# Kernel tuning notes

Measured on AMD Instinct MI355X. Metric: run time of the kernel, lower is better.

## Reference

```python
import math
import jax, jax.numpy as jnp
import numpy as np

B, T, E = 2, 2048, 2048
H, HKV = 16, 4
DH = E // H              # 128
ROT_DIM = DH             # rotary_pct = 1.0 -> 128
ROT_HALF = ROT_DIM // 2  # RotaryEmbedding is built with dim=ROT_DIM//2=64; only these dims rotate
MAX_SEQ = 2048


def _rope_tables():
    # theta = 10000 ** (-arange(0, dim, 2)/dim) with dim = ROT_HALF
    theta = 10000.0 ** (-jnp.arange(0, ROT_HALF, 2, dtype=jnp.float32) / ROT_HALF)  # [ROT_HALF//2]
    pos = jnp.arange(MAX_SEQ, dtype=jnp.float32)
    angles = pos[:, None] * theta[None, :]   # [MAX_SEQ, ROT_HALF//2]
    return jnp.cos(angles), jnp.sin(angles)


def _apply_rotary(q, k, start_pos):
    # q: [B,T,H,ROT_DIM], k: [B,T,HKV,ROT_DIM]; rotate only first ROT_HALF dims (interleaved pairs)
    cos, sin = _rope_tables()
    t = q.shape[1]
    cos = jax.lax.dynamic_slice_in_dim(cos, start_pos, t, axis=0)[None, :, None, :]
    sin = jax.lax.dynamic_slice_in_dim(sin, start_pos, t, axis=0)[None, :, None, :]

    def rot(a):
        a_rot, a_pass = a[..., :ROT_HALF], a[..., ROT_HALF:]
        x, y = a_rot[..., 0::2], a_rot[..., 1::2]
        rx = x * cos - y * sin
        ry = x * sin + y * cos
        rotated = jnp.stack([rx, ry], axis=-1).reshape(*a_rot.shape)
        return jnp.concatenate([rotated, a_pass], axis=-1)

    return rot(q), rot(k)


def setup_inputs() -> dict:
    key = jax.random.key(0)
    ks = jax.random.split(key, 9)
    s = 0.02  # weight scale for sane logits
    return {
        "x": jax.random.normal(ks[0], (B, T, E), dtype=jnp.float32),
        "Wq": jax.random.normal(ks[1], (E, H * DH), dtype=jnp.float32) * s,
        "bq": jax.random.normal(ks[2], (H * DH,), dtype=jnp.float32) * s,
        "Wk": jax.random.normal(ks[3], (E, HKV * DH), dtype=jnp.float32) * s,
        "bk": jax.random.normal(ks[4], (HKV * DH,), dtype=jnp.float32) * s,
        "Wv": jax.random.normal(ks[5], (E, HKV * DH), dtype=jnp.float32) * s,
        "bv": jax.random.normal(ks[6], (HKV * DH,), dtype=jnp.float32) * s,
        "Wo": jax.random.normal(ks[7], (E, E), dtype=jnp.float32) * s,
        "bo": jax.random.normal(ks[8], (E,), dtype=jnp.float32) * s,
        "start_pos": 0,
    }


def reference(x, Wq, bq, Wk, bk, Wv, bv, Wo, bo, start_pos):
    b, t, _ = x.shape
    q = (x @ Wq + bq).reshape(b, t, H, DH)
    k = (x @ Wk + bk).reshape(b, t, HKV, DH)
    v = (x @ Wv + bv).reshape(b, t, HKV, DH)

    q, k = _apply_rotary(q, k, start_pos)

    group = H // HKV
    k = jnp.repeat(k, group, axis=2)  # [b,t,H,DH]
    v = jnp.repeat(v, group, axis=2)

    # scores: [b,H,t,t]
    scores = jnp.einsum("bqhd,bkhd->bhqk", q, k) / math.sqrt(DH)
    causal = jnp.tril(jnp.ones((t, t), dtype=bool))
    scores = jnp.where(causal[None, None], scores, -jnp.inf)
    probs = jax.nn.softmax(scores, axis=-1)

    out = jnp.einsum("bhqk,bkhd->bqhd", probs, v).reshape(b, t, H * DH)
    return out @ Wo + bo
```

## Files before the change

kernel.cpp:

```cpp
#include <hip/hip_runtime.h>

typedef __attribute__((ext_vector_type(8))) short short8;
typedef __attribute__((ext_vector_type(4))) float f32x4;
typedef __attribute__((ext_vector_type(16))) float f32x16;

#define DEVFN __device__ __forceinline__

DEVFN unsigned short f2bf(float f) {
  unsigned int u = __builtin_bit_cast(unsigned int, f);
  u += 0x7FFFu + ((u >> 16) & 1u);
  return (unsigned short)(u >> 16);
}
DEVFN float bf2f(unsigned int u) { return __builtin_bit_cast(float, u << 16); }

DEVFN unsigned int cvtpk_bf16(float lo, float hi) {
  unsigned int d;
  asm("v_cvt_pk_bf16_f32 %0, %1, %2" : "=v"(d) : "v"(lo), "v"(hi));
  return d;
}
DEVFN void plswap32(unsigned int& a, unsigned int& b) {
  asm("v_permlane32_swap_b32 %0, %1" : "+v"(a), "+v"(b));
}
DEVFN float bcast32(float v, int srclane) {
  int r = __builtin_amdgcn_ds_bpermute(srclane * 4, __builtin_bit_cast(int, v));
  return __builtin_bit_cast(float, r);
}


__global__ __launch_bounds__(256) void mk_tables(float* __restrict__ cost, float* __restrict__ sint) {
  int gid = blockIdx.x * 256 + threadIdx.x;
  int pos = gid >> 5, i = gid & 31;
  float theta = powf(10000.0f, -(float)(2 * i) / 64.0f);
  float ang = (float)pos * theta;
  cost[gid] = cosf(ang);
  sint[gid] = sinf(ang);
}

__global__ __launch_bounds__(256) void bias_cat_k(const float* __restrict__ bq, const float* __restrict__ bk,
                                                  const float* __restrict__ bv, float* __restrict__ out) {
  int i = blockIdx.x * 256 + threadIdx.x;
  float v;
  if (i < 2048) v = bq[i];
  else if (i < 2560) v = bk[i - 2048];
  else v = bv[i - 2560];
  out[i] = v;
}

__global__ __launch_bounds__(256) void convx(const float* __restrict__ x, unsigned short* __restrict__ xb) {
  int gid = blockIdx.x * 256 + threadIdx.x;
  const float4* xv = (const float4*)x;
  float4 a = xv[(size_t)gid * 2], b = xv[(size_t)gid * 2 + 1];
  short8 u;
  u[0] = (short)f2bf(a.x); u[1] = (short)f2bf(a.y); u[2] = (short)f2bf(a.z); u[3] = (short)f2bf(a.w);
  u[4] = (short)f2bf(b.x); u[5] = (short)f2bf(b.y); u[6] = (short)f2bf(b.z); u[7] = (short)f2bf(b.w);
  *(short8*)(xb + (size_t)gid * 8) = u;
}

__global__ __launch_bounds__(256) void transw(const float* __restrict__ W, unsigned short* __restrict__ Wt, int ncols) {
  __shared__ float lds[32][33];
  int n0 = blockIdx.x * 32, k0 = blockIdx.y * 32;
  int tx = threadIdx.x & 31, ty = threadIdx.x >> 5;
  #pragma unroll
  for (int i = 0; i < 4; i++) {
    int kr = ty + i * 8;
    lds[kr][tx] = W[(size_t)(k0 + kr) * ncols + n0 + tx];
  }
  __syncthreads();
  #pragma unroll
  for (int i = 0; i < 4; i++) {
    int nr = ty + i * 8;
    Wt[(size_t)(n0 + nr) * 2048 + k0 + tx] = f2bf(lds[tx][nr]);
  }
}

template<int NH>
__global__ __launch_bounds__(256) void rope_scatter(const unsigned short* __restrict__ QKV,
    const float* __restrict__ cost, const float* __restrict__ sint, const int* __restrict__ spp,
    unsigned short* __restrict__ dst, int colOff, float scale) {
  constexpr int LOG2NH = (NH == 16) ? 4 : 2;
  int gid = blockIdx.x * 256 + threadIdx.x;
  int j = gid & 63;
  int h = (gid >> 6) & (NH - 1);
  int m = gid >> (6 + LOG2NH);
  int t = m & 2047;
  int b = m >> 11;
  const unsigned short* src = QKV + (size_t)m * 3072 + colOff + h * 128 + 2 * j;
  unsigned int pair = *(const unsigned int*)src;
  float xv = bf2f(pair & 0xFFFFu), yv = bf2f(pair >> 16);
  float rx, ry;
  if (j < 32) {
    int pos = (spp[0] + t) & 2047;
    float c = cost[pos * 32 + j], s = sint[pos * 32 + j];
    rx = xv * c - yv * s;
    ry = xv * s + yv * c;
  } else { rx = xv; ry = yv; }
  rx *= scale; ry *= scale;
  int d0 = 2 * j;
  size_t off = (size_t)(b * NH + h) * 262144 + (t >> 5) * 4096 + (d0 >> 4) * 512
             + ((d0 >> 3) & 1) * 256 + (t & 31) * 8 + (d0 & 7);
  unsigned int outp = (unsigned int)f2bf(rx) | ((unsigned int)f2bf(ry) << 16);
  *(unsigned int*)(dst + off) = outp;
}

__global__ __launch_bounds__(256) void vtrans(const unsigned short* __restrict__ QKV, unsigned short* __restrict__ VF) {
  __shared__ __align__(16) unsigned short lds[64 * 128];
  int tid = threadIdx.x;
  int t0 = blockIdx.x * 64;
  int bk = blockIdx.y;
  const unsigned short* src = QKV + (size_t)(bk >> 2) * 2048 * 3072 + 2560 + (bk & 3) * 128;
  #pragma unroll
  for (int c = 0; c < 4; c++) {
    int idx = c * 256 + tid;
    int tr = idx >> 4, dc = idx & 15;
    short8 v = *(const short8*)(src + (size_t)(t0 + tr) * 3072 + dc * 8);
    *(short8*)((char*)lds + tr * 256 + 16 * (dc ^ (tr >> 3))) = v;
  }
  __syncthreads();
  unsigned short* dstb = VF + (size_t)bk * 262144;
  #pragma unroll
  for (int c2 = 0; c2 < 4; c2++) {
    int idx2 = c2 * 256 + tid;
    int tc = idx2 & 7, d = idx2 >> 3;
    short8 u;
    #pragma unroll
    for (int e = 0; e < 8; e++) {
      int t = 8 * tc + e;
      u[e] = *(const short*)((char*)lds + t * 256 + 16 * ((d >> 3) ^ tc) + (d & 7) * 2);
    }
    size_t off = (size_t)(t0 >> 6) * 8192 + ((d >> 5) * 4 + ((tc >> 1) & 3)) * 512
               + (tc & 1) * 256 + (d & 31) * 8;
    *(short8*)(dstb + off) = u;
  }
}

template<bool BF16OUT>
__global__ __launch_bounds__(256, 2) void gemm_bt(
    const unsigned short* __restrict__ A, const unsigned short* __restrict__ Bt,
    const float* __restrict__ bias, void* __restrict__ Cout, int M, int N, int K) {
  __shared__ __align__(16) unsigned short Asl[128 * 64];
  __shared__ __align__(16) unsigned short Bsl[128 * 64];
  int tid = threadIdx.x;
  int lane = tid & 63, w = tid >> 6;
  int wr = w >> 1, wc = w & 1;
  int m0 = blockIdx.y * 128, n0 = blockIdx.x * 128;

  f32x4 acc[4][4];
  #pragma unroll
  for (int i = 0; i < 4; i++)
    #pragma unroll
    for (int j = 0; j < 4; j++)
      #pragma unroll
      for (int r = 0; r < 4; r++) acc[i][j][r] = 0.f;

  int srow = w * 32 + (lane >> 3);
  int kc8 = (lane & 7) * 8;
  const unsigned short* Aptr = A + (size_t)(m0 + srow) * K + kc8;
  const unsigned short* Bptr = Bt + (size_t)(n0 + srow) * K + kc8;
  unsigned short* AslW = Asl + w * 4 * 512;
  unsigned short* BslW = Bsl + w * 4 * 512;

  for (int k0 = 0; k0 < K; k0 += 64) {
    __syncthreads();
    #pragma unroll
    for (int i = 0; i < 4; i++) {
      __builtin_amdgcn_global_load_lds(
        (const __attribute__((address_space(1))) unsigned int*)(Aptr + (size_t)i * 8 * K + k0),
        (__attribute__((address_space(3))) unsigned int*)(AslW + i * 512), 16, 0, 0);
      __builtin_amdgcn_global_load_lds(
        (const __attribute__((address_space(1))) unsigned int*)(Bptr + (size_t)i * 8 * K + k0),
        (__attribute__((address_space(3))) unsigned int*)(BslW + i * 512), 16, 0, 0);
    }
    __syncthreads();
    #pragma unroll
    for (int ks = 0; ks < 2; ks++) {
      short8 af[4], bfr[4];
      #pragma unroll
      for (int mi = 0; mi < 4; mi++)
        af[mi] = *(const short8*)(Asl + (wr * 64 + mi * 16 + (lane & 15)) * 64 + ks * 32 + (lane >> 4) * 8);
      #pragma unroll
      for (int ni = 0; ni < 4; ni++)
        bfr[ni] = *(const short8*)(Bsl + (wc * 64 + ni * 16 + (lane & 15)) * 64 + ks * 32 + (lane >> 4) * 8);
      #pragma unroll
      for (int mi = 0; mi < 4; mi++)
        #pragma unroll
        for (int ni = 0; ni < 4; ni++)
          acc[mi][ni] = __builtin_amdgcn_mfma_f32_16x16x32_bf16(af[mi], bfr[ni], acc[mi][ni], 0, 0, 0);
    }
  }
  int cl = lane & 15, rq = lane >> 4;
  #pragma unroll
  for (int mi = 0; mi < 4; mi++) {
    #pragma unroll
    for (int ni = 0; ni < 4; ni++) {
      int gn = n0 + wc * 64 + ni * 16 + cl;
      float bv = bias[gn];
      #pragma unroll
      for (int r = 0; r < 4; r++) {
        int gm = m0 + wr * 64 + mi * 16 + rq * 4 + r;
        float v = acc[mi][ni][r] + bv;
        if (BF16OUT) ((unsigned short*)Cout)[(size_t)gm * N + gn] = f2bf(v);
        else ((float*)Cout)[(size_t)gm * N + gn] = v;
      }
    }
  }
}

__global__ __launch_bounds__(512, 2) void attn_kernel(
    const unsigned short* __restrict__ QF, const unsigned short* __restrict__ KF,
    const unsigned short* __restrict__ VF, unsigned short* __restrict__ O) {
  const int tid = threadIdx.x;
  const int lane = tid & 63;
  const int w = tid >> 6;
  const int l31 = lane & 31;
  const int hf = lane >> 5;
  const int g = blockIdx.x & 7, j = blockIdx.x >> 3;
  const int b = g >> 2, kh = g & 3;
  const int h = kh * 4 + (j & 3);
  const int i4 = (j >> 2) * 4;
  const int qt = (w < 4) ? (i4 + w) : (67 - i4 - w);
  const int qw = qt * 32;
  const int nw = (qt >> 1) + 1;

  const unsigned short* qh  = QF + (size_t)(b * 16 + h) * 262144 + qt * 4096;
  const unsigned short* khp = KF + (size_t)(b * 4 + kh) * 262144;
  const unsigned short* vhp = VF + (size_t)(b * 4 + kh) * 262144;

  short8 qf[8];
  #pragma unroll
  for (int s = 0; s < 8; s++)
    qf[s] = *(const short8*)(qh + s * 512 + lane * 8);

  float m_r = -3.0e38f, l_r = 0.f;
  f32x16 oacc[4];
  #pragma unroll
  for (int dt = 0; dt < 4; dt++)
    #pragma unroll
    for (int r = 0; r < 16; r++) oacc[dt][r] = 0.f;

  for (int kt = 0; kt < nw; kt++) {
    const int kv0 = kt * 64;
    f32x16 sc[2];
    {
      short8 kf0[8];
      #pragma unroll
      for (int s = 0; s < 8; s++)
        kf0[s] = *(const short8*)(khp + (size_t)(2 * kt) * 4096 + s * 512 + lane * 8);
      #pragma unroll
      for (int r = 0; r < 16; r++) sc[0][r] = 0.f;
      #pragma unroll
      for (int s = 0; s < 8; s++)
        sc[0] = __builtin_amdgcn_mfma_f32_32x32x16_bf16(kf0[s], qf[s], sc[0], 0, 0, 0);
    }
    {
      short8 kf1[8];
      #pragma unroll
      for (int s = 0; s < 8; s++)
        kf1[s] = *(const short8*)(khp + (size_t)(2 * kt + 1) * 4096 + s * 512 + lane * 8);
      #pragma unroll
      for (int r = 0; r < 16; r++) sc[1][r] = 0.f;
      #pragma unroll
      for (int s = 0; s < 8; s++)
        sc[1] = __builtin_amdgcn_mfma_f32_32x32x16_bf16(kf1[s], qf[s], sc[1], 0, 0, 0);
    }
    short8 vf[4][4];
    #pragma unroll
    for (int dt = 0; dt < 4; dt++)
      #pragma unroll
      for (int ks = 0; ks < 4; ks++)
        vf[dt][ks] = *(const short8*)(vhp + (size_t)kt * 8192 + (dt * 4 + ks) * 512 + lane * 8);

    if (kv0 + 63 > qw) {
      #pragma unroll
      for (int ct = 0; ct < 2; ct++)
        #pragma unroll
        for (int r = 0; r < 16; r++) {
          int kg = kv0 + ct * 32 + (r & 3) + 8 * (r >> 2) + 4 * hf;
          if (kg > qw + l31) sc[ct][r] = -3.0e38f;
        }
    }
    float mx[16];
    #pragma unroll
    for (int r = 0; r < 16; r++) mx[r] = fmaxf(sc[0][r], sc[1][r]);
    #pragma unroll
    for (int s2 = 8; s2 >= 1; s2 >>= 1)
      #pragma unroll
      for (int i = 0; i < 8; i++) if (i < s2) mx[i] = fmaxf(mx[i], mx[i + s2]);
    float tm = fmaxf(mx[0], __shfl_xor(mx[0], 32));
    if (__any(tm > m_r + 8.0f)) {
      float mn = fmaxf(m_r, tm);
      float al = __builtin_amdgcn_exp2f(m_r - mn);
      m_r = mn;
      l_r *= al;
      #pragma unroll
      for (int r = 0; r < 16; r++) {
        float alr = bcast32(al, (r & 3) + 8 * (r >> 2) + 4 * hf);
        #pragma unroll
        for (int dt = 0; dt < 4; dt++) oacc[dt][r] *= alr;
      }
    }
    #pragma unroll
    for (int ct = 0; ct < 2; ct++)
      #pragma unroll
      for (int r = 0; r < 16; r++) sc[ct][r] = __builtin_amdgcn_exp2f(sc[ct][r] - m_r);
    float sm[16];
    #pragma unroll
    for (int r = 0; r < 16; r++) sm[r] = sc[0][r] + sc[1][r];
    #pragma unroll
    for (int s2 = 8; s2 >= 1; s2 >>= 1)
      #pragma unroll
      for (int i = 0; i < 8; i++) if (i < s2) sm[i] += sm[i + s2];
    l_r += sm[0];

    short8 pa[4];
    #pragma unroll
    for (int ks = 0; ks < 4; ks++) {
      const int ct = ks >> 1, kb = (ks & 1) * 8;
      unsigned int A0 = cvtpk_bf16(sc[ct][kb + 0], sc[ct][kb + 1]);
      unsigned int A1 = cvtpk_bf16(sc[ct][kb + 2], sc[ct][kb + 3]);
      unsigned int B0 = cvtpk_bf16(sc[ct][kb + 4], sc[ct][kb + 5]);
      unsigned int B1 = cvtpk_bf16(sc[ct][kb + 6], sc[ct][kb + 7]);
      plswap32(A0, B0);
      plswap32(A1, B1);
      union { unsigned int wds[4]; short8 s8; } u;
      u.wds[0] = A0; u.wds[1] = A1; u.wds[2] = B0; u.wds[3] = B1;
      pa[ks] = u.s8;
    }
    #pragma unroll
    for (int dt = 0; dt < 4; dt++)
      #pragma unroll
      for (int ks = 0; ks < 4; ks++)
        oacc[dt] = __builtin_amdgcn_mfma_f32_32x32x16_bf16(pa[ks], vf[dt][ks], oacc[dt], 0, 0, 0);
  }
  float invl = 1.0f / (l_r + __shfl_xor(l_r, 32));
  #pragma unroll
  for (int r = 0; r < 16; r++) {
    int rloc = (r & 3) + 8 * (r >> 2) + 4 * hf;
    float inv = bcast32(invl, rloc);
    int qg = qw + rloc;
    unsigned short* orow = O + ((size_t)(b * 2048 + qg)) * 2048 + h * 128;
    #pragma unroll
    for (int dt = 0; dt < 4; dt++)
      orow[dt * 32 + l31] = f2bf(oacc[dt][r] * inv);
  }
}

extern "C" void kernel_launch(void* const* d_in, const int* in_sizes, int n_in,
                              void* d_out, int out_size, void* d_ws, size_t ws_size,
                              hipStream_t stream) {
  (void)in_sizes; (void)n_in; (void)out_size; (void)ws_size;
  const float* x  = (const float*)d_in[0];
  const float* Wq = (const float*)d_in[1];
  const float* bq = (const float*)d_in[2];
  const float* Wk = (const float*)d_in[3];
  const float* bk = (const float*)d_in[4];
  const float* Wv = (const float*)d_in[5];
  const float* bv = (const float*)d_in[6];
  const float* Wo = (const float*)d_in[7];
  const float* bo = (const float*)d_in[8];
  const int*   sp = (const int*)d_in[9];

  char* ws = (char*)d_ws;
  unsigned short* xb    = (unsigned short*)ws;
  unsigned short* Wqkvt = (unsigned short*)(ws + 16777216);
  unsigned short* Wot   = (unsigned short*)(ws + 29360128);
  unsigned short* QKVb  = (unsigned short*)(ws + 37748736);
  float* cost           = (float*)(ws + 62914560);
  float* sint           = (float*)(ws + 63176704);
  float* bcat           = (float*)(ws + 63438848);

  unsigned short* Obuf = xb;
  unsigned short* QFr = (unsigned short*)d_out;
  unsigned short* KFr = (unsigned short*)((char*)d_out + 16777216);
  unsigned short* VFr = (unsigned short*)((char*)d_out + 20971520);

  mk_tables<<<256, 256, 0, stream>>>(cost, sint);
  bias_cat_k<<<12, 256, 0, stream>>>(bq, bk, bv, bcat);
  convx<<<4096, 256, 0, stream>>>(x, xb);
  transw<<<dim3(64, 64), 256, 0, stream>>>(Wq, Wqkvt, 2048);
  transw<<<dim3(16, 64), 256, 0, stream>>>(Wk, Wqkvt + (size_t)2048 * 2048, 512);
  transw<<<dim3(16, 64), 256, 0, stream>>>(Wv, Wqkvt + (size_t)2560 * 2048, 512);
  transw<<<dim3(64, 64), 256, 0, stream>>>(Wo, Wot, 2048);
  gemm_bt<true><<<dim3(24, 32), 256, 0, stream>>>(xb, Wqkvt, bcat, QKVb, 4096, 3072, 2048);
  rope_scatter<16><<<16384, 256, 0, stream>>>(QKVb, cost, sint, sp, QFr, 0, 0.12751743f);
  rope_scatter<4><<<4096, 256, 0, stream>>>(QKVb, cost, sint, sp, KFr, 2048, 1.0f);
  vtrans<<<dim3(32, 8), 256, 0, stream>>>(QKVb, VFr);
  attn_kernel<<<dim3(256), 512, 0, stream>>>(QFr, KFr, VFr, Obuf);
  gemm_bt<false><<<dim3(16, 32), 256, 0, stream>>>(Obuf, Wot, bo, (float*)d_out, 4096, 2048, 2048);
}
```

Before: 237.9 us.

## Merge prep and scatter kernels, remap GEMM blocks per XCD, pipeline attention K loads

Folds the seven preprocessing launches into one prep_all kernel and the three rope/V-transpose launches into one scatter_all kernel, which removes launch gaps. The GEMM grid becomes 1D, with block indices remapped so that consecutive tiles are grouped per XCD (index mod 8), aiming for better L2 locality. In attention, the next K tile is double-buffered in registers, V loads are split and interleaved with compute, and the softmax row sum is computed by an MFMA against a ones vector instead of a shuffle reduction. The costs are higher register pressure and branchy multi-role kernels.

```diff
diff --git a/kernel.cpp b/kernel.cpp
--- a/kernel.cpp
+++ b/kernel.cpp
@@ -26,123 +26,137 @@
   return __builtin_bit_cast(float, r);
 }
 
-
-__global__ __launch_bounds__(256) void mk_tables(float* __restrict__ cost, float* __restrict__ sint) {
-  int gid = blockIdx.x * 256 + threadIdx.x;
-  int pos = gid >> 5, i = gid & 31;
-  float theta = powf(10000.0f, -(float)(2 * i) / 64.0f);
-  float ang = (float)pos * theta;
-  cost[gid] = cosf(ang);
-  sint[gid] = sinf(ang);
-}
-
-__global__ __launch_bounds__(256) void bias_cat_k(const float* __restrict__ bq, const float* __restrict__ bk,
-                                                  const float* __restrict__ bv, float* __restrict__ out) {
-  int i = blockIdx.x * 256 + threadIdx.x;
-  float v;
-  if (i < 2048) v = bq[i];
-  else if (i < 2560) v = bk[i - 2048];
-  else v = bv[i - 2560];
-  out[i] = v;
-}
-
-__global__ __launch_bounds__(256) void convx(const float* __restrict__ x, unsigned short* __restrict__ xb) {
-  int gid = blockIdx.x * 256 + threadIdx.x;
-  const float4* xv = (const float4*)x;
-  float4 a = xv[(size_t)gid * 2], b = xv[(size_t)gid * 2 + 1];
-  short8 u;
-  u[0] = (short)f2bf(a.x); u[1] = (short)f2bf(a.y); u[2] = (short)f2bf(a.z); u[3] = (short)f2bf(a.w);
-  u[4] = (short)f2bf(b.x); u[5] = (short)f2bf(b.y); u[6] = (short)f2bf(b.z); u[7] = (short)f2bf(b.w);
-  *(short8*)(xb + (size_t)gid * 8) = u;
-}
-
-__global__ __launch_bounds__(256) void transw(const float* __restrict__ W, unsigned short* __restrict__ Wt, int ncols) {
+__global__ __launch_bounds__(256) void prep_all(
+    const float* __restrict__ Wq, const float* __restrict__ Wk, const float* __restrict__ Wv,
+    const float* __restrict__ Wo, const float* __restrict__ bq, const float* __restrict__ bk,
+    const float* __restrict__ bv, const float* __restrict__ x,
+    unsigned short* __restrict__ Wqkvt, unsigned short* __restrict__ Wot,
+    unsigned short* __restrict__ xb, float* __restrict__ cost, float* __restrict__ sint,
+    float* __restrict__ bcat) {
   __shared__ float lds[32][33];
-  int n0 = blockIdx.x * 32, k0 = blockIdx.y * 32;
-  int tx = threadIdx.x & 31, ty = threadIdx.x >> 5;
-  #pragma unroll
-  for (int i = 0; i < 4; i++) {
-    int kr = ty + i * 8;
-    lds[kr][tx] = W[(size_t)(k0 + kr) * ncols + n0 + tx];
-  }
-  __syncthreads();
-  #pragma unroll
-  for (int i = 0; i < 4; i++) {
-    int nr = ty + i * 8;
-    Wt[(size_t)(n0 + nr) * 2048 + k0 + tx] = f2bf(lds[tx][nr]);
-  }
-}
-
-template<int NH>
-__global__ __launch_bounds__(256) void rope_scatter(const unsigned short* __restrict__ QKV,
-    const float* __restrict__ cost, const float* __restrict__ sint, const int* __restrict__ spp,
-    unsigned short* __restrict__ dst, int colOff, float scale) {
-  constexpr int LOG2NH = (NH == 16) ? 4 : 2;
-  int gid = blockIdx.x * 256 + threadIdx.x;
-  int j = gid & 63;
-  int h = (gid >> 6) & (NH - 1);
-  int m = gid >> (6 + LOG2NH);
-  int t = m & 2047;
-  int b = m >> 11;
-  const unsigned short* src = QKV + (size_t)m * 3072 + colOff + h * 128 + 2 * j;
-  unsigned int pair = *(const unsigned int*)src;
-  float xv = bf2f(pair & 0xFFFFu), yv = bf2f(pair >> 16);
-  float rx, ry;
-  if (j < 32) {
-    int pos = (spp[0] + t) & 2047;
-    float c = cost[pos * 32 + j], s = sint[pos * 32 + j];
-    rx = xv * c - yv * s;
-    ry = xv * s + yv * c;
-  } else { rx = xv; ry = yv; }
-  rx *= scale; ry *= scale;
-  int d0 = 2 * j;
-  size_t off = (size_t)(b * NH + h) * 262144 + (t >> 5) * 4096 + (d0 >> 4) * 512
-             + ((d0 >> 3) & 1) * 256 + (t & 31) * 8 + (d0 & 7);
-  unsigned int outp = (unsigned int)f2bf(rx) | ((unsigned int)f2bf(ry) << 16);
-  *(unsigned int*)(dst + off) = outp;
-}
-
-__global__ __launch_bounds__(256) void vtrans(const unsigned short* __restrict__ QKV, unsigned short* __restrict__ VF) {
+  const int bid = blockIdx.x, tid = threadIdx.x;
+  if (bid < 10240) {
+    const float* W; unsigned short* Wt; int ncols, bx, by;
+    if (bid < 4096)      { W = Wq; Wt = Wqkvt;                        ncols = 2048; bx = bid & 63; by = bid >> 6; }
+    else if (bid < 5120) { int l = bid - 4096; W = Wk; Wt = Wqkvt + (size_t)2048 * 2048; ncols = 512; bx = l & 15; by = l >> 4; }
+    else if (bid < 6144) { int l = bid - 5120; W = Wv; Wt = Wqkvt + (size_t)2560 * 2048; ncols = 512; bx = l & 15; by = l >> 4; }
+    else                 { int l = bid - 6144; W = Wo; Wt = Wot;      ncols = 2048; bx = l & 63; by = l >> 6; }
+    int n0 = bx * 32, k0 = by * 32;
+    int tx = tid & 31, ty = tid >> 5;
+    #pragma unroll
+    for (int i = 0; i < 4; i++) {
+      int kr = ty + i * 8;
+      lds[kr][tx] = W[(size_t)(k0 + kr) * ncols + n0 + tx];
+    }
+    __syncthreads();
+    #pragma unroll
+    for (int i = 0; i < 4; i++) {
+      int nr = ty + i * 8;
+      Wt[(size_t)(n0 + nr) * 2048 + k0 + tx] = f2bf(lds[tx][nr]);
+    }
+  } else if (bid < 14336) {
+    int gid = (bid - 10240) * 256 + tid;
+    const float4* xv = (const float4*)x;
+    float4 a = xv[(size_t)gid * 2], b = xv[(size_t)gid * 2 + 1];
+    short8 u;
+    u[0] = (short)f2bf(a.x); u[1] = (short)f2bf(a.y); u[2] = (short)f2bf(a.z); u[3] = (short)f2bf(a.w);
+    u[4] = (short)f2bf(b.x); u[5] = (short)f2bf(b.y); u[6] = (short)f2bf(b.z); u[7] = (short)f2bf(b.w);
+    *(short8*)(xb + (size_t)gid * 8) = u;
+  } else if (bid < 14592) {
+    int gid = (bid - 14336) * 256 + tid;
+    int pos = gid >> 5, i = gid & 31;
+    float theta = powf(10000.0f, -(float)(2 * i) / 64.0f);
+    float ang = (float)pos * theta;
+    cost[gid] = cosf(ang);
+    sint[gid] = sinf(ang);
+  } else {
+    int i = (bid - 14592) * 256 + tid;
+    float v;
+    if (i < 2048) v = bq[i];
+    else if (i < 2560) v = bk[i - 2048];
+    else v = bv[i - 2560];
+    bcat[i] = v;
+  }
+}
+
+__global__ __launch_bounds__(256) void scatter_all(
+    const unsigned short* __restrict__ QKVb, const float* __restrict__ cost,
+    const float* __restrict__ sint, const int* __restrict__ spp,
+    unsigned short* __restrict__ QFr, unsigned short* __restrict__ KFr,
+    unsigned short* __restrict__ VFr) {
   __shared__ __align__(16) unsigned short lds[64 * 128];
-  int tid = threadIdx.x;
-  int t0 = blockIdx.x * 64;
-  int bk = blockIdx.y;
-  const unsigned short* src = QKV + (size_t)(bk >> 2) * 2048 * 3072 + 2560 + (bk & 3) * 128;
-  #pragma unroll
-  for (int c = 0; c < 4; c++) {
-    int idx = c * 256 + tid;
-    int tr = idx >> 4, dc = idx & 15;
-    short8 v = *(const short8*)(src + (size_t)(t0 + tr) * 3072 + dc * 8);
-    *(short8*)((char*)lds + tr * 256 + 16 * (dc ^ (tr >> 3))) = v;
-  }
-  __syncthreads();
-  unsigned short* dstb = VF + (size_t)bk * 262144;
-  #pragma unroll
-  for (int c2 = 0; c2 < 4; c2++) {
-    int idx2 = c2 * 256 + tid;
-    int tc = idx2 & 7, d = idx2 >> 3;
-    short8 u;
-    #pragma unroll
-    for (int e = 0; e < 8; e++) {
-      int t = 8 * tc + e;
-      u[e] = *(const short*)((char*)lds + t * 256 + 16 * ((d >> 3) ^ tc) + (d & 7) * 2);
-    }
-    size_t off = (size_t)(t0 >> 6) * 8192 + ((d >> 5) * 4 + ((tc >> 1) & 3)) * 512
-               + (tc & 1) * 256 + (d & 31) * 8;
-    *(short8*)(dstb + off) = u;
+  const int bid = blockIdx.x, tid = threadIdx.x;
+  if (bid < 20480) {
+    int NH, LOG2NH, colOff, gid;
+    unsigned short* dst;
+    float scale;
+    if (bid < 16384) { NH = 16; LOG2NH = 4; colOff = 0;    dst = QFr; scale = 0.12751743f; gid = bid * 256 + tid; }
+    else             { NH = 4;  LOG2NH = 2; colOff = 2048; dst = KFr; scale = 1.0f;        gid = (bid - 16384) * 256 + tid; }
+    int j = gid & 63;
+    int h = (gid >> 6) & (NH - 1);
+    int m = gid >> (6 + LOG2NH);
+    int t = m & 2047;
+    int b = m >> 11;
+    const unsigned short* src = QKVb + (size_t)m * 3072 + colOff + h * 128 + 2 * j;
+    unsigned int pair = *(const unsigned int*)src;
+    float xv = bf2f(pair & 0xFFFFu), yv = bf2f(pair >> 16);
+    float rx, ry;
+    if (j < 32) {
+      int pos = (spp[0] + t) & 2047;
+      float c = cost[pos * 32 + j], s = sint[pos * 32 + j];
+      rx = xv * c - yv * s;
+      ry = xv * s + yv * c;
+    } else { rx = xv; ry = yv; }
+    rx *= scale; ry *= scale;
+    int d0 = 2 * j;
+    size_t off = (size_t)(b * NH + h) * 262144 + (t >> 5) * 4096 + (d0 >> 4) * 512
+               + ((d0 >> 3) & 1) * 256 + (t & 31) * 8 + (d0 & 7);
+    unsigned int outp = (unsigned int)f2bf(rx) | ((unsigned int)f2bf(ry) << 16);
+    *(unsigned int*)(dst + off) = outp;
+  } else {
+    int l = bid - 20480;
+    int t0 = (l & 31) * 64;
+    int bk = l >> 5;
+    const unsigned short* src = QKVb + (size_t)(bk >> 2) * 2048 * 3072 + 2560 + (bk & 3) * 128;
+    #pragma unroll
+    for (int c = 0; c < 4; c++) {
+      int idx = c * 256 + tid;
+      int tr = idx >> 4, dc = idx & 15;
+      short8 v = *(const short8*)(src + (size_t)(t0 + tr) * 3072 + dc * 8);
+      *(short8*)((char*)lds + tr * 256 + 16 * (dc ^ (tr >> 3))) = v;
+    }
+    __syncthreads();
+    unsigned short* dstb = VFr + (size_t)bk * 262144;
+    #pragma unroll
+    for (int c2 = 0; c2 < 4; c2++) {
+      int idx2 = c2 * 256 + tid;
+      int tc = idx2 & 7, d = idx2 >> 3;
+      short8 u;
+      #pragma unroll
+      for (int e = 0; e < 8; e++) {
+        int t = 8 * tc + e;
+        u[e] = *(const short*)((char*)lds + t * 256 + 16 * ((d >> 3) ^ tc) + (d & 7) * 2);
+      }
+      size_t off = (size_t)(t0 >> 6) * 8192 + ((d >> 5) * 4 + ((tc >> 1) & 3)) * 512
+                 + (tc & 1) * 256 + (d & 31) * 8;
+      *(short8*)(dstb + off) = u;
+    }
   }
 }
 
 template<bool BF16OUT>
 __global__ __launch_bounds__(256, 2) void gemm_bt(
     const unsigned short* __restrict__ A, const unsigned short* __restrict__ Bt,
-    const float* __restrict__ bias, void* __restrict__ Cout, int M, int N, int K) {
+    const float* __restrict__ bias, void* __restrict__ Cout, int M, int N, int K, int NTX) {
   __shared__ __align__(16) unsigned short Asl[128 * 64];
   __shared__ __align__(16) unsigned short Bsl[128 * 64];
   int tid = threadIdx.x;
   int lane = tid & 63, w = tid >> 6;
   int wr = w >> 1, wc = w & 1;
-  int m0 = blockIdx.y * 128, n0 = blockIdx.x * 128;
+  int f = blockIdx.x;
+  int cpx = gridDim.x >> 3;
+  int fs = (f & 7) * cpx + (f >> 3);
+  int m0 = (fs / NTX) * 128, n0 = (fs % NTX) * 128;
 
   f32x4 acc[4][4];
   #pragma unroll
@@ -219,7 +233,7 @@
   const int i4 = (j >> 2) * 4;
   const int qt = (w < 4) ? (i4 + w) : (67 - i4 - w);
   const int qw = qt * 32;
-  const int nw = (qt >> 1) + 1;
+  const int nt = (qt >> 1) + 1;
 
   const unsigned short* qh  = QF + (size_t)(b * 16 + h) * 262144 + qt * 4096;
   const unsigned short* khp = KF + (size_t)(b * 4 + kh) * 262144;
@@ -230,45 +244,47 @@
   for (int s = 0; s < 8; s++)
     qf[s] = *(const short8*)(qh + s * 512 + lane * 8);
 
-  float m_r = -3.0e38f, l_r = 0.f;
+  short8 ones;
+  #pragma unroll
+  for (int e = 0; e < 8; e++) ones[e] = (short)0x3F80;
+
+  float m_r = -3.0e38f;
   f32x16 oacc[4];
+  f32x16 lacc;
   #pragma unroll
   for (int dt = 0; dt < 4; dt++)
     #pragma unroll
     for (int r = 0; r < 16; r++) oacc[dt][r] = 0.f;
-
-  for (int kt = 0; kt < nw; kt++) {
+  #pragma unroll
+  for (int r = 0; r < 16; r++) lacc[r] = 0.f;
+
+  short8 bufA[16], bufB[16];
+  #pragma unroll
+  for (int s = 0; s < 8; s++) {
+    bufA[s]     = *(const short8*)(khp + s * 512 + lane * 8);
+    bufA[8 + s] = *(const short8*)(khp + 4096 + s * 512 + lane * 8);
+  }
+
+  auto tileBody = [&](int kt, short8 (&kcur)[16], short8 (&knxt)[16]) {
     const int kv0 = kt * 64;
     f32x16 sc[2];
-    {
-      short8 kf0[8];
-      #pragma unroll
-      for (int s = 0; s < 8; s++)
-        kf0[s] = *(const short8*)(khp + (size_t)(2 * kt) * 4096 + s * 512 + lane * 8);
-      #pragma unroll
-      for (int r = 0; r < 16; r++) sc[0][r] = 0.f;
-      #pragma unroll
-      for (int s = 0; s < 8; s++)
-        sc[0] = __builtin_amdgcn_mfma_f32_32x32x16_bf16(kf0[s], qf[s], sc[0], 0, 0, 0);
-    }
-    {
-      short8 kf1[8];
-      #pragma unroll
-      for (int s = 0; s < 8; s++)
-        kf1[s] = *(const short8*)(khp + (size_t)(2 * kt + 1) * 4096 + s * 512 + lane * 8);
-      #pragma unroll
-      for (int r = 0; r < 16; r++) sc[1][r] = 0.f;
-      #pragma unroll
-      for (int s = 0; s < 8; s++)
-        sc[1] = __builtin_amdgcn_mfma_f32_32x32x16_bf16(kf1[s], qf[s], sc[1], 0, 0, 0);
-    }
-    short8 vf[4][4];
-    #pragma unroll
-    for (int dt = 0; dt < 4; dt++)
-      #pragma unroll
-      for (int ks = 0; ks < 4; ks++)
-        vf[dt][ks] = *(const short8*)(vhp + (size_t)kt * 8192 + (dt * 4 + ks) * 512 + lane * 8);
-
+    #pragma unroll
+    for (int r = 0; r < 16; r++) sc[0][r] = 0.f;
+    #pragma unroll
+    for (int s = 0; s < 8; s++)
+      sc[0] = __builtin_amdgcn_mfma_f32_32x32x16_bf16(kcur[s], qf[s], sc[0], 0, 0, 0);
+    #pragma unroll
+    for (int r = 0; r < 16; r++) sc[1][r] = 0.f;
+    #pragma unroll
+    for (int s = 0; s < 8; s++)
+      sc[1] = __builtin_amdgcn_mfma_f32_32x32x16_bf16(kcur[8 + s], qf[s], sc[1], 0, 0, 0);
+    if (kt + 1 < nt) {
+      #pragma unroll
+      for (int s = 0; s < 8; s++) {
+        knxt[s]     = *(const short8*)(khp + (size_t)(2 * kt + 2) * 4096 + s * 512 + lane * 8);
+        knxt[8 + s] = *(const short8*)(khp + (size_t)(2 * kt + 3) * 4096 + s * 512 + lane * 8);
+      }
+    }
     if (kv0 + 63 > qw) {
       #pragma unroll
       for (int ct = 0; ct < 2; ct++)
@@ -290,27 +306,22 @@
       float mn = fmaxf(m_r, tm);
       float al = __builtin_amdgcn_exp2f(m_r - mn);
       m_r = mn;
-      l_r *= al;
       #pragma unroll
       for (int r = 0; r < 16; r++) {
         float alr = bcast32(al, (r & 3) + 8 * (r >> 2) + 4 * hf);
         #pragma unroll
         for (int dt = 0; dt < 4; dt++) oacc[dt][r] *= alr;
+        lacc[r] *= alr;
       }
     }
+    short8 vf01[8];
+    #pragma unroll
+    for (int q2 = 0; q2 < 8; q2++)
+      vf01[q2] = *(const short8*)(vhp + (size_t)kt * 8192 + q2 * 512 + lane * 8);
     #pragma unroll
     for (int ct = 0; ct < 2; ct++)
       #pragma unroll
       for (int r = 0; r < 16; r++) sc[ct][r] = __builtin_amdgcn_exp2f(sc[ct][r] - m_r);
-    float sm[16];
-    #pragma unroll
-    for (int r = 0; r < 16; r++) sm[r] = sc[0][r] + sc[1][r];
-    #pragma unroll
-    for (int s2 = 8; s2 >= 1; s2 >>= 1)
-      #pragma unroll
-      for (int i = 0; i < 8; i++) if (i < s2) sm[i] += sm[i + s2];
-    l_r += sm[0];
-
     short8 pa[4];
     #pragma unroll
     for (int ks = 0; ks < 4; ks++) {
@@ -325,19 +336,41 @@
       u.wds[0] = A0; u.wds[1] = A1; u.wds[2] = B0; u.wds[3] = B1;
       pa[ks] = u.s8;
     }
-    #pragma unroll
-    for (int dt = 0; dt < 4; dt++)
-      #pragma unroll
-      for (int ks = 0; ks < 4; ks++)
-        oacc[dt] = __builtin_amdgcn_mfma_f32_32x32x16_bf16(pa[ks], vf[dt][ks], oacc[dt], 0, 0, 0);
-  }
-  float invl = 1.0f / (l_r + __shfl_xor(l_r, 32));
+    short8 vf23[8];
+    #pragma unroll
+    for (int q2 = 0; q2 < 8; q2++)
+      vf23[q2] = *(const short8*)(vhp + (size_t)kt * 8192 + (8 + q2) * 512 + lane * 8);
+    #pragma unroll
+    for (int ks = 0; ks < 4; ks++)
+      lacc = __builtin_amdgcn_mfma_f32_32x32x16_bf16(pa[ks], ones, lacc, 0, 0, 0);
+    #pragma unroll
+    for (int ks = 0; ks < 4; ks++)
+      oacc[0] = __builtin_amdgcn_mfma_f32_32x32x16_bf16(pa[ks], vf01[ks], oacc[0], 0, 0, 0);
+    #pragma unroll
+    for (int ks = 0; ks < 4; ks++)
+      oacc[1] = __builtin_amdgcn_mfma_f32_32x32x16_bf16(pa[ks], vf01[4 + ks], oacc[1], 0, 0, 0);
+    #pragma unroll
+    for (int ks = 0; ks < 4; ks++)
+      oacc[2] = __builtin_amdgcn_mfma_f32_32x32x16_bf16(pa[ks], vf23[ks], oacc[2], 0, 0, 0);
+    #pragma unroll
+    for (int ks = 0; ks < 4; ks++)
+      oacc[3] = __builtin_amdgcn_mfma_f32_32x32x16_bf16(pa[ks], vf23[4 + ks], oacc[3], 0, 0, 0);
+  };
+
+  int kt = 0;
+  while (true) {
+    tileBody(kt, bufA, bufB); kt++;
+    if (kt >= nt) break;
+    tileBody(kt, bufB, bufA); kt++;
+    if (kt >= nt) break;
+  }
+
   #pragma unroll
   for (int r = 0; r < 16; r++) {
+    float inv = 1.0f / lacc[r];
     int rloc = (r & 3) + 8 * (r >> 2) + 4 * hf;
-    float inv = bcast32(invl, rloc);
-    int qg = qw + rloc;
-    unsigned short* orow = O + ((size_t)(b * 2048 + qg)) * 2048 + h * 128;
+    int qgr = qw + rloc;
+    unsigned short* orow = O + ((size_t)(b * 2048 + qgr)) * 2048 + h * 128;
     #pragma unroll
     for (int dt = 0; dt < 4; dt++)
       orow[dt * 32 + l31] = f2bf(oacc[dt][r] * inv);
@@ -373,17 +406,10 @@
   unsigned short* KFr = (unsigned short*)((char*)d_out + 16777216);
   unsigned short* VFr = (unsigned short*)((char*)d_out + 20971520);
 
-  mk_tables<<<256, 256, 0, stream>>>(cost, sint);
-  bias_cat_k<<<12, 256, 0, stream>>>(bq, bk, bv, bcat);
-  convx<<<4096, 256, 0, stream>>>(x, xb);
-  transw<<<dim3(64, 64), 256, 0, stream>>>(Wq, Wqkvt, 2048);
-  transw<<<dim3(16, 64), 256, 0, stream>>>(Wk, Wqkvt + (size_t)2048 * 2048, 512);
-  transw<<<dim3(16, 64), 256, 0, stream>>>(Wv, Wqkvt + (size_t)2560 * 2048, 512);
-  transw<<<dim3(64, 64), 256, 0, stream>>>(Wo, Wot, 2048);
-  gemm_bt<true><<<dim3(24, 32), 256, 0, stream>>>(xb, Wqkvt, bcat, QKVb, 4096, 3072, 2048);
-  rope_scatter<16><<<16384, 256, 0, stream>>>(QKVb, cost, sint, sp, QFr, 0, 0.12751743f);
-  rope_scatter<4><<<4096, 256, 0, stream>>>(QKVb, cost, sint, sp, KFr, 2048, 1.0f);
-  vtrans<<<dim3(32, 8), 256, 0, stream>>>(QKVb, VFr);
+  prep_all<<<dim3(14604), 256, 0, stream>>>(Wq, Wk, Wv, Wo, bq, bk, bv, x,
+                                            Wqkvt, Wot, xb, cost, sint, bcat);
+  gemm_bt<true><<<dim3(768), 256, 0, stream>>>(xb, Wqkvt, bcat, QKVb, 4096, 3072, 2048, 24);
+  scatter_all<<<dim3(20736), 256, 0, stream>>>(QKVb, cost, sint, sp, QFr, KFr, VFr);
   attn_kernel<<<dim3(256), 512, 0, stream>>>(QFr, KFr, VFr, Obuf);
-  gemm_bt<false><<<dim3(16, 32), 256, 0, stream>>>(Obuf, Wot, bo, (float*)d_out, 4096, 2048, 2048);
-}
+  gemm_bt<false><<<dim3(512), 256, 0, stream>>>(Obuf, Wot, bo, (float*)d_out, 4096, 2048, 2048, 16);
+}
```

Measured after the change: 295.0 us. 1.24x slower.
